# Performance work log

Measured on AMD Instinct MI355X. Metric: run time of the kernel, lower is better.

The kernel has to match this reference:

```python
import jax, jax.numpy as jnp
import numpy as np

B, N, D, H, K = 256, 196, 768, 256, 8
NEG = -1e9


def setup_inputs() -> dict:
    key = jax.random.key(0)
    ks = jax.random.split(key, 7)
    s_in = 1.0 / np.sqrt(D)
    s_h = 1.0 / np.sqrt(H)
    return {
        "region_features": jax.random.normal(ks[0], (B, N, D), dtype=jnp.float32),
        "Wn": jax.random.uniform(ks[1], (D, H), jnp.float32, -s_in, s_in),
        "bn": jax.random.uniform(ks[2], (H,), jnp.float32, -s_in, s_in),
        "Wm": jax.random.uniform(ks[3], (H, H), jnp.float32, -s_h, s_h),
        "bm": jax.random.uniform(ks[4], (H,), jnp.float32, -s_h, s_h),
        "Wo": jax.random.uniform(ks[5], (H, D), jnp.float32, -s_h, s_h),
        "bo": jax.random.uniform(ks[6], (D,), jnp.float32, -s_h, s_h),
    }


def reference(region_features, Wn, bn, Wm, bm, Wo, bo):
    b, n, d = region_features.shape
    h = Wn.shape[1]
    nodes = jnp.einsum("bnd,dh->bnh", region_features, Wn) + bn        # [B,N,H]
    sim = jnp.einsum("bnh,bmh->bnm", nodes, nodes)                      # [B,N,N]
    sim = sim + jnp.eye(n, dtype=sim.dtype) * NEG                       # mask self
    k = min(K, n - 1)
    topk_vals, topk_idx = jax.lax.top_k(sim, k)                         # [B,N,k]
    # gather neighbor node features: nodes[b, topk_idx[b,n,k]]
    flat_idx = topk_idx.reshape(b, n * k)                               # [B,N*k]
    neigh = jnp.take_along_axis(nodes, flat_idx[:, :, None], axis=1)    # [B,N*k,H]
    neighs = neigh.reshape(b, n, k, h).mean(axis=2)                     # [B,N,H]
    msgs = jax.nn.relu(jnp.einsum("bnh,hg->bng", neighs, Wm) + bm)      # [B,N,H]
    updated = nodes + msgs
    out = jnp.einsum("bnh,hd->bnd", updated, Wo) + bo                   # [B,N,D]
    return (out, topk_vals)
```

## Files before the change

### kernel.cpp

```cpp
#include <hip/hip_runtime.h>


#define NN 196
#define MM 208
#define DD 768
#define HH 256

typedef unsigned short u16;
typedef __attribute__((ext_vector_type(8))) short short8;
typedef __attribute__((ext_vector_type(4))) float f32x4;

#define GLD16(gp, lp) __builtin_amdgcn_global_load_lds( \
    (__attribute__((address_space(1))) const void*)(gp), \
    (__attribute__((address_space(3))) void*)(lp), 16, 0, 0)

__device__ __forceinline__ u16 f2b(float f) {
  union { float f; unsigned int i; } c; c.f = f;
  unsigned int x = c.i;
  return (u16)((x + 0x7fffu + ((x >> 16) & 1u)) >> 16);
}
__device__ __forceinline__ float b2f(u16 u) {
  union { float f; unsigned int i; } c; c.i = ((unsigned int)u) << 16; return c.f;
}

__global__ __launch_bounds__(256) void transpose_w(
    const float* __restrict__ in, u16* __restrict__ out, int R, int C)
{
  __shared__ u16 tile[32][33];
  int bx = blockIdx.x, by = blockIdx.y;
  int t = threadIdx.x;
  int i = t >> 5, j = t & 31;
  #pragma unroll
  for (int s = 0; s < 32; s += 8)
    tile[i + s][j] = f2b(in[(size_t)(by * 32 + i + s) * C + bx * 32 + j]);
  __syncthreads();
  #pragma unroll
  for (int s = 0; s < 32; s += 8)
    out[(size_t)(bx * 32 + i + s) * R + by * 32 + j] = tile[j][i + s];
}

__global__ __launch_bounds__(1024, 4) void fused_batch(
    const float* __restrict__ X, const u16* __restrict__ WnT,
    const float* __restrict__ bn, const u16* __restrict__ WmT,
    const float* __restrict__ bm, const u16* __restrict__ WoT,
    const float* __restrict__ bo, u16* __restrict__ updatedG,
    float* __restrict__ outG, float* __restrict__ valsG)
{
  extern __shared__ __align__(16) u16 smem[];
  u16* nodesS = smem;
  u16* Xbuf0 = smem + 53248;
  u16* Xbuf1 = smem + 53248 + 6656;
  float* simS0 = (float*)(smem + 53248);
  float* simS1 = (float*)(smem + 53248 + 6656);
  u16* neighS0 = smem + 53248 + 13312;
  u16* neighS1 = smem + 53248 + 13312 + 4096;

  const int t = threadIdx.x;
  const int w = t >> 6;
  const int lane = t & 63;
  const int l15 = lane & 15;
  const int kg = lane >> 4;
  const int b = blockIdx.x;
  const float* Xb = X + (size_t)b * (NN * DD);
  u16* updGb = updatedG + (size_t)b * MM * HH;

  f32x4 acc[13];
  #pragma unroll
  for (int fr = 0; fr < 13; ++fr) acc[fr] = (f32x4)0.0f;

  const bool xact = (t < 832);
  const int xrow = t >> 2;
  const int xr2 = (xrow < NN) ? xrow : (NN - 1);
  const int xcb = (t & 3) * 8;
  const int xsw = (xrow >> 1) & 3;
  const int xj0 = t & 3;

  f32x4 xsA[2], xsB[2], xsC[2];
  short8 bfrC0, bfrN0;

#define S1_ISSUE(SET, KT) do { \
    const float* xp_ = Xb + (size_t)xr2 * DD + (KT) * 32 + xcb; \
    SET[0] = *(const f32x4*)(xp_); SET[1] = *(const f32x4*)(xp_ + 4); \
  } while (0)

#define S1_COMMIT(SET, BUFW) do { \
    short8 v_; \
    _Pragma("unroll") for (int q_ = 0; q_ < 8; ++q_) v_[q_] = (short)f2b(SET[q_ >> 2][q_ & 3]); \
    *(short8*)((BUFW) + xrow * 32 + ((xj0 ^ xsw) << 3)) = v_; \
  } while (0)

#define S1_STEP(KT, XI, XC, BUFR, BUFW) do { \
    if (xact && (KT) + 3 < 24) S1_ISSUE(XI, (KT) + 3); \
    if ((KT) + 1 < 24) \
      bfrN0 = *(const short8*)(WnT + (size_t)(w * 16 + l15) * DD + ((KT) + 1) * 32 + kg * 8); \
    __builtin_amdgcn_s_setprio(1); \
    _Pragma("unroll") for (int fr_ = 0; fr_ < 13; ++fr_) { \
      const int r_ = fr_ * 16 + l15; \
      short8 a_ = *(const short8*)((BUFR) + r_ * 32 + ((kg ^ ((r_ >> 1) & 3)) << 3)); \
      acc[fr_] = __builtin_amdgcn_mfma_f32_16x16x32_bf16(a_, bfrC0, acc[fr_], 0, 0, 0); \
    } \
    __builtin_amdgcn_s_setprio(0); \
    if (xact && (KT) + 1 < 24) S1_COMMIT(XC, BUFW); \
    __syncthreads(); \
    bfrC0 = bfrN0; \
  } while (0)

  if (xact) { S1_ISSUE(xsA, 0); S1_ISSUE(xsB, 1); S1_ISSUE(xsC, 2); S1_COMMIT(xsA, Xbuf0); }
  bfrC0 = *(const short8*)(WnT + (size_t)(w * 16 + l15) * DD + kg * 8);
  __syncthreads();

  for (int kb = 0; kb < 24; kb += 6) {
    S1_STEP(kb + 0, xsA, xsB, Xbuf0, Xbuf1);
    S1_STEP(kb + 1, xsB, xsC, Xbuf1, Xbuf0);
    S1_STEP(kb + 2, xsC, xsA, Xbuf0, Xbuf1);
    S1_STEP(kb + 3, xsA, xsB, Xbuf1, Xbuf0);
    S1_STEP(kb + 4, xsB, xsC, Xbuf0, Xbuf1);
    S1_STEP(kb + 5, xsC, xsA, Xbuf1, Xbuf0);
  }

  {
    const float bnv = bn[w * 16 + l15];
    #pragma unroll
    for (int fr = 0; fr < 13; ++fr)
      #pragma unroll
      for (int ri = 0; ri < 4; ++ri) {
        const int r = fr * 16 + kg * 4 + ri;
        const int c = w * 16 + l15;
        nodesS[r * 256 + (((c >> 3) ^ (r & 7)) << 3) + (c & 7)] = f2b(acc[fr][ri] + bnv);
      }
  }
  __syncthreads();

  const float bmv = bm[w * 16 + l15];

  for (int s = 0; s < 13; ++s) {
    float* simSp = (s & 1) ? simS1 : simS0;
    u16* neighSp = (s & 1) ? neighS1 : neighS0;

    if (w < 13) {
      f32x4 s0 = (f32x4)0.0f;
      __builtin_amdgcn_s_setprio(1);
      #pragma unroll
      for (int kt = 0; kt < 8; ++kt) {
        const int ar = s * 16 + l15;
        const int ja = kt * 4 + kg;
        short8 av = *(const short8*)(nodesS + ar * 256 + ((ja ^ (ar & 7)) << 3));
        const int br = w * 16 + l15;
        short8 bv = *(const short8*)(nodesS + br * 256 + ((ja ^ (br & 7)) << 3));
        s0 = __builtin_amdgcn_mfma_f32_16x16x32_bf16(av, bv, s0, 0, 0, 0);
      }
      __builtin_amdgcn_s_setprio(0);
      #pragma unroll
      for (int ri = 0; ri < 4; ++ri) simSp[(kg * 4 + ri) * MM + w * 16 + l15] = s0[ri];
    }
    __syncthreads();

    {
      const int lr = w;
      const int n = s * 16 + lr;
      if (n < NN) {
        const float* srow = simSp + lr * MM;
        unsigned int v[4];
        #pragma unroll
        for (int i = 0; i < 4; ++i) {
          const int c = i * 64 + lane;
          const float f = (c < NN && c != n) ? srow[c] : -1e30f;
          union { float f; unsigned int i; } cv; cv.f = f;
          const unsigned int u = cv.i;
          const unsigned int key = u ^ ((u & 0x80000000u) ? 0xFFFFFFFFu : 0x80000000u);
          v[i] = (key & 0xFFFFFF00u) | (255u - (unsigned int)c);
        }
        int kcol[8];
        #pragma unroll
        for (int it = 0; it < 8; ++it) {
          unsigned int p0 = v[0] > v[1] ? v[0] : v[1];
          unsigned int p1 = v[2] > v[3] ? v[2] : v[3];
          unsigned int pk = p0 > p1 ? p0 : p1;
          #pragma unroll
          for (int off = 32; off >= 1; off >>= 1) {
            const unsigned int o = (unsigned int)__shfl_xor((int)pk, off);
            pk = o > pk ? o : pk;
          }
          const int cm = 255 - (int)(pk & 255u);
          kcol[it] = cm;
          if (lane == 0) {
            const unsigned int key = pk & 0xFFFFFF00u;
            union { float f; unsigned int i; } rv;
            rv.i = (key & 0x80000000u) ? (key ^ 0x80000000u) : ~key;
            valsG[((size_t)b * NN + n) * 8 + it] = rv.f;
          }
          if (lane == (cm & 63)) v[cm >> 6] = 0u;
        }
        float a0 = 0.f, a1 = 0.f, a2 = 0.f, a3 = 0.f;
        #pragma unroll
        for (int j = 0; j < 8; ++j) {
          const int kr = kcol[j];
          const uint2 u = *(const uint2*)(nodesS + kr * 256 + (((lane >> 1) ^ (kr & 7)) << 3) + (lane & 1) * 4);
          a0 += b2f((u16)(u.x & 0xffff)); a1 += b2f((u16)(u.x >> 16));
          a2 += b2f((u16)(u.y & 0xffff)); a3 += b2f((u16)(u.y >> 16));
        }
        const int jN = lane >> 1;
        u16* np = neighSp + lr * 256 + ((jN ^ (lr & 7)) << 3) + (lane & 1) * 4;
        np[0] = f2b(a0 * 0.125f); np[1] = f2b(a1 * 0.125f);
        np[2] = f2b(a2 * 0.125f); np[3] = f2b(a3 * 0.125f);
      }
    }
    __syncthreads();

    {
      f32x4 m0 = (f32x4)0.0f;
      __builtin_amdgcn_s_setprio(1);
      #pragma unroll
      for (int kt = 0; kt < 8; ++kt) {
        const int ja = kt * 4 + kg;
        short8 a = *(const short8*)(neighSp + l15 * 256 + ((ja ^ (l15 & 7)) << 3));
        short8 b0 = *(const short8*)(WmT + (size_t)(w * 16 + l15) * HH + kt * 32 + kg * 8);
        m0 = __builtin_amdgcn_mfma_f32_16x16x32_bf16(a, b0, m0, 0, 0, 0);
      }
      __builtin_amdgcn_s_setprio(0);
      #pragma unroll
      for (int ri = 0; ri < 4; ++ri) {
        const int r = s * 16 + kg * 4 + ri;
        const int c = w * 16 + l15;
        const float mv = m0[ri] + bmv;
        const float nodev = b2f(nodesS[r * 256 + (((c >> 3) ^ (r & 7)) << 3) + (c & 7)]);
        updGb[(size_t)r * HH + c] = f2b(nodev + fmaxf(mv, 0.0f));
      }
    }
  }

  __syncthreads();
  #pragma unroll
  for (int q = 0; q < 7; ++q) {
    const int si = q * 1024 + t;
    if (si < 6656) {
      const int r = si >> 5;
      const int jj = si & 31;
      const int j = jj ^ (r & 7);
      GLD16(updGb + (size_t)r * HH + j * 8, nodesS + si * 8);
    }
  }
  __syncthreads();

  for (int ch = 0; ch < 3; ++ch) {
    f32x4 oacc[13];
    #pragma unroll
    for (int fr = 0; fr < 13; ++fr) oacc[fr] = (f32x4)0.0f;
    __builtin_amdgcn_s_setprio(1);
    #pragma unroll
    for (int kt = 0; kt < 8; ++kt) {
      short8 bfr = *(const short8*)(WoT + (size_t)(ch * 256 + w * 16 + l15) * HH + kt * 32 + kg * 8);
      #pragma unroll
      for (int fr = 0; fr < 13; ++fr) {
        const int r = fr * 16 + l15;
        const int ja = kt * 4 + kg;
        short8 a = *(const short8*)(nodesS + r * 256 + ((ja ^ (r & 7)) << 3));
        oacc[fr] = __builtin_amdgcn_mfma_f32_16x16x32_bf16(a, bfr, oacc[fr], 0, 0, 0);
      }
    }
    __builtin_amdgcn_s_setprio(0);
    const float bov = bo[ch * 256 + w * 16 + l15];
    #pragma unroll
    for (int fr = 0; fr < 13; ++fr)
      #pragma unroll
      for (int ri = 0; ri < 4; ++ri) {
        const int r = fr * 16 + kg * 4 + ri;
        if (r < NN)
          outG[((size_t)b * NN + r) * DD + ch * 256 + w * 16 + l15] =
              oacc[fr][ri] + bov;
      }
  }
}

extern "C" void kernel_launch(void* const* d_in, const int* in_sizes, int n_in,
                              void* d_out, int out_size, void* d_ws, size_t ws_size,
                              hipStream_t stream) {
  const float* X  = (const float*)d_in[0];
  const float* Wn = (const float*)d_in[1];
  const float* bn = (const float*)d_in[2];
  const float* Wm = (const float*)d_in[3];
  const float* bm = (const float*)d_in[4];
  const float* Wo = (const float*)d_in[5];
  const float* bo = (const float*)d_in[6];

  char* p = (char*)d_ws;
  u16* WnT = (u16*)p;  p += (size_t)256 * 768 * 2;
  u16* WmT = (u16*)p;  p += (size_t)256 * 256 * 2;
  u16* WoT = (u16*)p;  p += (size_t)768 * 256 * 2;
  u16* updatedG = (u16*)p;  p += (size_t)256 * MM * HH * 2;

  float* out  = (float*)d_out;
  float* vals = out + (size_t)256 * NN * DD;

  transpose_w<<<dim3(256 / 32, 768 / 32), 256, 0, stream>>>(Wn, WnT, 768, 256);
  transpose_w<<<dim3(256 / 32, 256 / 32), 256, 0, stream>>>(Wm, WmT, 256, 256);
  transpose_w<<<dim3(768 / 32, 256 / 32), 256, 0, stream>>>(Wo, WoT, 256, 768);

  const int smem_bytes = 149504;
  (void)hipFuncSetAttribute((const void*)fused_batch,
                            hipFuncAttributeMaxDynamicSharedMemorySize, smem_bytes);
  fused_batch<<<256, 1024, smem_bytes, stream>>>(X, WnT, bn, WmT, bm, WoT, bo,
                                                 updatedG, out, vals);
}
```

Before: 169.9 us.

## Split fused batch kernel into nodes GEMM, graph strips, and output GEMM kernels

The single per-batch fused kernel is split into three launches: a node-projection GEMM writing bf16 nodes to global memory, a graph kernel that loads nodes, computes similarity/top-k/messages and writes the updated features, and a separate output GEMM that tiles 64-row slabs across 832 blocks. The aim is to stop one large, shared-memory-heavy, 256-block kernel from being limited by occupancy and serialization. Each phase can use its own shared-memory footprint, and the output projection gets more parallel blocks. In exchange, the nodes tensor takes an extra global write and read, and two more kernel launches are added.

```diff
diff --git a/kernel.cpp b/kernel.cpp
--- a/kernel.cpp
+++ b/kernel.cpp
@@ -39,21 +39,12 @@
     out[(size_t)(bx * 32 + i + s) * R + by * 32 + j] = tile[j][i + s];
 }
 
-__global__ __launch_bounds__(1024, 4) void fused_batch(
+__global__ __launch_bounds__(1024, 4) void nodes_gemm(
     const float* __restrict__ X, const u16* __restrict__ WnT,
-    const float* __restrict__ bn, const u16* __restrict__ WmT,
-    const float* __restrict__ bm, const u16* __restrict__ WoT,
-    const float* __restrict__ bo, u16* __restrict__ updatedG,
-    float* __restrict__ outG, float* __restrict__ valsG)
+    const float* __restrict__ bn, u16* __restrict__ nodesG)
 {
-  extern __shared__ __align__(16) u16 smem[];
-  u16* nodesS = smem;
-  u16* Xbuf0 = smem + 53248;
-  u16* Xbuf1 = smem + 53248 + 6656;
-  float* simS0 = (float*)(smem + 53248);
-  float* simS1 = (float*)(smem + 53248 + 6656);
-  u16* neighS0 = smem + 53248 + 13312;
-  u16* neighS1 = smem + 53248 + 13312 + 4096;
+  __shared__ __align__(16) u16 Xbuf0[6656];
+  __shared__ __align__(16) u16 Xbuf1[6656];
 
   const int t = threadIdx.x;
   const int w = t >> 6;
@@ -62,7 +53,6 @@
   const int kg = lane >> 4;
   const int b = blockIdx.x;
   const float* Xb = X + (size_t)b * (NN * DD);
-  u16* updGb = updatedG + (size_t)b * MM * HH;
 
   f32x4 acc[13];
   #pragma unroll
@@ -119,6 +109,7 @@
   }
 
   {
+    u16* ndst = nodesG + (size_t)b * (MM * HH);
     const float bnv = bn[w * 16 + l15];
     #pragma unroll
     for (int fr = 0; fr < 13; ++fr)
@@ -126,8 +117,41 @@
       for (int ri = 0; ri < 4; ++ri) {
         const int r = fr * 16 + kg * 4 + ri;
         const int c = w * 16 + l15;
-        nodesS[r * 256 + (((c >> 3) ^ (r & 7)) << 3) + (c & 7)] = f2b(acc[fr][ri] + bnv);
-      }
+        ndst[(size_t)r * HH + c] = f2b(acc[fr][ri] + bnv);
+      }
+  }
+}
+
+__global__ __launch_bounds__(1024, 4) void graph_strips(
+    const u16* __restrict__ nodesG, const u16* __restrict__ WmT,
+    const float* __restrict__ bm, u16* __restrict__ updatedG,
+    float* __restrict__ valsG)
+{
+  extern __shared__ __align__(16) u16 smem[];
+  u16* nodesS = smem;
+  float* simS0 = (float*)(smem + 53248);
+  float* simS1 = (float*)(smem + 53248 + 6656);
+  u16* neighS0 = smem + 53248 + 13312;
+  u16* neighS1 = smem + 53248 + 13312 + 4096;
+
+  const int t = threadIdx.x;
+  const int w = t >> 6;
+  const int lane = t & 63;
+  const int l15 = lane & 15;
+  const int kg = lane >> 4;
+  const int b = blockIdx.x;
+  const u16* nodesGb = nodesG + (size_t)b * (MM * HH);
+  u16* updGb = updatedG + (size_t)b * MM * HH;
+
+  #pragma unroll
+  for (int q = 0; q < 7; ++q) {
+    const int si = q * 1024 + t;
+    if (si < 6656) {
+      const int r = si >> 5;
+      const int jj = si & 31;
+      const int j = jj ^ (r & 7);
+      GLD16(nodesGb + (size_t)r * HH + j * 8, nodesS + si * 8);
+    }
   }
   __syncthreads();
 
@@ -228,45 +252,58 @@
       }
     }
   }
-
+}
+
+__global__ __launch_bounds__(1024, 8) void out_gemm(
+    const u16* __restrict__ updatedG, const u16* __restrict__ WoT,
+    const float* __restrict__ bo, float* __restrict__ outG)
+{
+  __shared__ __align__(16) u16 aS[64 * 256];
+
+  const int t = threadIdx.x;
+  const int w = t >> 6;
+  const int lane = t & 63;
+  const int l15 = lane & 15;
+  const int kg = lane >> 4;
+  const int row0 = blockIdx.x * 64;
+
+  #pragma unroll
+  for (int q = 0; q < 2; ++q) {
+    const int si = q * 1024 + t;
+    const int r = si >> 5;
+    const int jj = si & 31;
+    const int j = jj ^ (r & 7);
+    GLD16(updatedG + (size_t)(row0 + r) * HH + j * 8, aS + si * 8);
+  }
   __syncthreads();
-  #pragma unroll
-  for (int q = 0; q < 7; ++q) {
-    const int si = q * 1024 + t;
-    if (si < 6656) {
-      const int r = si >> 5;
-      const int jj = si & 31;
-      const int j = jj ^ (r & 7);
-      GLD16(updGb + (size_t)r * HH + j * 8, nodesS + si * 8);
-    }
-  }
-  __syncthreads();
 
   for (int ch = 0; ch < 3; ++ch) {
-    f32x4 oacc[13];
+    f32x4 oacc[4];
     #pragma unroll
-    for (int fr = 0; fr < 13; ++fr) oacc[fr] = (f32x4)0.0f;
+    for (int fr = 0; fr < 4; ++fr) oacc[fr] = (f32x4)0.0f;
     __builtin_amdgcn_s_setprio(1);
     #pragma unroll
     for (int kt = 0; kt < 8; ++kt) {
       short8 bfr = *(const short8*)(WoT + (size_t)(ch * 256 + w * 16 + l15) * HH + kt * 32 + kg * 8);
       #pragma unroll
-      for (int fr = 0; fr < 13; ++fr) {
+      for (int fr = 0; fr < 4; ++fr) {
         const int r = fr * 16 + l15;
         const int ja = kt * 4 + kg;
-        short8 a = *(const short8*)(nodesS + r * 256 + ((ja ^ (r & 7)) << 3));
+        short8 a = *(const short8*)(aS + r * 256 + ((ja ^ (r & 7)) << 3));
         oacc[fr] = __builtin_amdgcn_mfma_f32_16x16x32_bf16(a, bfr, oacc[fr], 0, 0, 0);
       }
     }
     __builtin_amdgcn_s_setprio(0);
     const float bov = bo[ch * 256 + w * 16 + l15];
     #pragma unroll
-    for (int fr = 0; fr < 13; ++fr)
+    for (int fr = 0; fr < 4; ++fr)
       #pragma unroll
       for (int ri = 0; ri < 4; ++ri) {
-        const int r = fr * 16 + kg * 4 + ri;
-        if (r < NN)
-          outG[((size_t)b * NN + r) * DD + ch * 256 + w * 16 + l15] =
+        const int rg = row0 + fr * 16 + kg * 4 + ri;
+        const int batch = rg / MM;
+        const int rl = rg - batch * MM;
+        if (rl < NN)
+          outG[((size_t)batch * NN + rl) * DD + ch * 256 + w * 16 + l15] =
               oacc[fr][ri] + bov;
       }
   }
@@ -287,6 +324,7 @@
   u16* WnT = (u16*)p;  p += (size_t)256 * 768 * 2;
   u16* WmT = (u16*)p;  p += (size_t)256 * 256 * 2;
   u16* WoT = (u16*)p;  p += (size_t)768 * 256 * 2;
+  u16* nodesG = (u16*)p;    p += (size_t)256 * MM * HH * 2;
   u16* updatedG = (u16*)p;  p += (size_t)256 * MM * HH * 2;
 
   float* out  = (float*)d_out;
@@ -296,9 +334,12 @@
   transpose_w<<<dim3(256 / 32, 256 / 32), 256, 0, stream>>>(Wm, WmT, 256, 256);
   transpose_w<<<dim3(768 / 32, 256 / 32), 256, 0, stream>>>(Wo, WoT, 256, 768);
 
+  nodes_gemm<<<256, 1024, 0, stream>>>(X, WnT, bn, nodesG);
+
   const int smem_bytes = 149504;
-  (void)hipFuncSetAttribute((const void*)fused_batch,
+  (void)hipFuncSetAttribute((const void*)graph_strips,
                             hipFuncAttributeMaxDynamicSharedMemorySize, smem_bytes);
-  fused_batch<<<256, 1024, smem_bytes, stream>>>(X, WnT, bn, WmT, bm, WoT, bo,
-                                                 updatedG, out, vals);
-}
+  graph_strips<<<256, 1024, smem_bytes, stream>>>(nodesG, WmT, bm, updatedG, vals);
+
+  out_gemm<<<832, 1024, 0, stream>>>(updatedG, WoT, bo, out);
+}
```

Result: slower. 517.3 us (+204.4%).

## Hoist sim B-fragments into registers and re-tile output GEMM by row blocks

Applied to the files above, without the earlier changes.

The similarity loop's B operand, which is the same for a given wave across all 13 row steps, is now loaded from LDS once into registers instead of every iteration. The output projection is reorganised so each of 13 waves owns a 16-row block of updated nodes, held in registers, and sweeps all 768 output columns in pairs of 16-column tiles. That second change removes the repeated LDS A-operand reads of the old column-split scheme, but it reads Wo from global memory per wave, leaves 3 of the 16 waves idle, and adds register pressure.

```diff
diff --git a/kernel.cpp b/kernel.cpp
--- a/kernel.cpp
+++ b/kernel.cpp
@@ -133,6 +133,16 @@
 
   const float bmv = bm[w * 16 + l15];
 
+  short8 bvh[8];
+  if (w < 13) {
+    const int br = w * 16 + l15;
+    #pragma unroll
+    for (int kt = 0; kt < 8; ++kt) {
+      const int ja = kt * 4 + kg;
+      bvh[kt] = *(const short8*)(nodesS + br * 256 + ((ja ^ (br & 7)) << 3));
+    }
+  }
+
   for (int s = 0; s < 13; ++s) {
     float* simSp = (s & 1) ? simS1 : simS0;
     u16* neighSp = (s & 1) ? neighS1 : neighS0;
@@ -145,9 +155,7 @@
         const int ar = s * 16 + l15;
         const int ja = kt * 4 + kg;
         short8 av = *(const short8*)(nodesS + ar * 256 + ((ja ^ (ar & 7)) << 3));
-        const int br = w * 16 + l15;
-        short8 bv = *(const short8*)(nodesS + br * 256 + ((ja ^ (br & 7)) << 3));
-        s0 = __builtin_amdgcn_mfma_f32_16x16x32_bf16(av, bv, s0, 0, 0, 0);
+        s0 = __builtin_amdgcn_mfma_f32_16x16x32_bf16(av, bvh[kt], s0, 0, 0, 0);
       }
       __builtin_amdgcn_s_setprio(0);
       #pragma unroll
@@ -242,33 +250,42 @@
   }
   __syncthreads();
 
-  for (int ch = 0; ch < 3; ++ch) {
-    f32x4 oacc[13];
-    #pragma unroll
-    for (int fr = 0; fr < 13; ++fr) oacc[fr] = (f32x4)0.0f;
-    __builtin_amdgcn_s_setprio(1);
-    #pragma unroll
-    for (int kt = 0; kt < 8; ++kt) {
-      short8 bfr = *(const short8*)(WoT + (size_t)(ch * 256 + w * 16 + l15) * HH + kt * 32 + kg * 8);
-      #pragma unroll
-      for (int fr = 0; fr < 13; ++fr) {
-        const int r = fr * 16 + l15;
-        const int ja = kt * 4 + kg;
-        short8 a = *(const short8*)(nodesS + r * 256 + ((ja ^ (r & 7)) << 3));
-        oacc[fr] = __builtin_amdgcn_mfma_f32_16x16x32_bf16(a, bfr, oacc[fr], 0, 0, 0);
-      }
-    }
-    __builtin_amdgcn_s_setprio(0);
-    const float bov = bo[ch * 256 + w * 16 + l15];
-    #pragma unroll
-    for (int fr = 0; fr < 13; ++fr)
+  if (w < 13) {
+    short8 avh[8];
+    {
+      const int r = w * 16 + l15;
+      #pragma unroll
+      for (int kt = 0; kt < 8; ++kt)
+        avh[kt] = *(const short8*)(nodesS + r * 256 + (((kt * 4 + kg) ^ (r & 7)) << 3));
+    }
+    const int orow = w * 16 + kg * 4;
+    float* outRowBase = outG + (size_t)b * NN * DD;
+
+    for (int ct2 = 0; ct2 < 24; ++ct2) {
+      const int c0 = ct2 * 32 + l15;
+      const int c1 = c0 + 16;
+      f32x4 acc0 = (f32x4)0.0f, acc1 = (f32x4)0.0f;
+      __builtin_amdgcn_s_setprio(1);
+      #pragma unroll
+      for (int kt = 0; kt < 8; ++kt) {
+        short8 b0 = *(const short8*)(WoT + (size_t)c0 * HH + kt * 32 + kg * 8);
+        short8 b1 = *(const short8*)(WoT + (size_t)c1 * HH + kt * 32 + kg * 8);
+        acc0 = __builtin_amdgcn_mfma_f32_16x16x32_bf16(avh[kt], b0, acc0, 0, 0, 0);
+        acc1 = __builtin_amdgcn_mfma_f32_16x16x32_bf16(avh[kt], b1, acc1, 0, 0, 0);
+      }
+      __builtin_amdgcn_s_setprio(0);
+      const float bo0 = bo[c0];
+      const float bo1 = bo[c1];
       #pragma unroll
       for (int ri = 0; ri < 4; ++ri) {
-        const int r = fr * 16 + kg * 4 + ri;
-        if (r < NN)
-          outG[((size_t)b * NN + r) * DD + ch * 256 + w * 16 + l15] =
-              oacc[fr][ri] + bov;
-      }
+        const int r = orow + ri;
+        if (r < NN) {
+          float* op = outRowBase + (size_t)r * DD + ct2 * 32 + l15;
+          op[0]  = acc0[ri] + bo0;
+          op[16] = acc1[ri] + bo1;
+        }
+      }
+    }
   }
 }
 
```

Measured after the change: 279.7 us. +64.6%, slower.

## Fuse output projection into per-strip message loop via LDS instead of global roundtrip

Applied to the files above, without the earlier changes.

Each 16-row strip's updated node features are now written to a small swizzled LDS buffer instead of a global workspace. The output projection (Wo GEMM) for that strip runs immediately inside the strip loop. Each wave covers three 16-column output tiles, so the separate reload phase and the final 3-chunk GEMM are gone. This removes the global write/readback of the updated tensor and two block barriers. The cost is an extra barrier per strip, more LDS, and Wo fragments reloaded from global memory for every strip rather than once per chunk.

```diff
diff --git a/kernel.cpp b/kernel.cpp
--- a/kernel.cpp
+++ b/kernel.cpp
@@ -9,10 +9,6 @@
 typedef unsigned short u16;
 typedef __attribute__((ext_vector_type(8))) short short8;
 typedef __attribute__((ext_vector_type(4))) float f32x4;
-
-#define GLD16(gp, lp) __builtin_amdgcn_global_load_lds( \
-    (__attribute__((address_space(1))) const void*)(gp), \
-    (__attribute__((address_space(3))) void*)(lp), 16, 0, 0)
 
 __device__ __forceinline__ u16 f2b(float f) {
   union { float f; unsigned int i; } c; c.f = f;
@@ -43,7 +39,7 @@
     const float* __restrict__ X, const u16* __restrict__ WnT,
     const float* __restrict__ bn, const u16* __restrict__ WmT,
     const float* __restrict__ bm, const u16* __restrict__ WoT,
-    const float* __restrict__ bo, u16* __restrict__ updatedG,
+    const float* __restrict__ bo,
     float* __restrict__ outG, float* __restrict__ valsG)
 {
   extern __shared__ __align__(16) u16 smem[];
@@ -54,6 +50,7 @@
   float* simS1 = (float*)(smem + 53248 + 6656);
   u16* neighS0 = smem + 53248 + 13312;
   u16* neighS1 = smem + 53248 + 13312 + 4096;
+  u16* updS    = smem + 53248 + 13312 + 8192;
 
   const int t = threadIdx.x;
   const int w = t >> 6;
@@ -62,7 +59,6 @@
   const int kg = lane >> 4;
   const int b = blockIdx.x;
   const float* Xb = X + (size_t)b * (NN * DD);
-  u16* updGb = updatedG + (size_t)b * MM * HH;
 
   f32x4 acc[13];
   #pragma unroll
@@ -221,54 +217,43 @@
       #pragma unroll
       for (int ri = 0; ri < 4; ++ri) {
         const int r = s * 16 + kg * 4 + ri;
+        const int rl = kg * 4 + ri;
         const int c = w * 16 + l15;
         const float mv = m0[ri] + bmv;
         const float nodev = b2f(nodesS[r * 256 + (((c >> 3) ^ (r & 7)) << 3) + (c & 7)]);
-        updGb[(size_t)r * HH + c] = f2b(nodev + fmaxf(mv, 0.0f));
-      }
-    }
-  }
-
-  __syncthreads();
-  #pragma unroll
-  for (int q = 0; q < 7; ++q) {
-    const int si = q * 1024 + t;
-    if (si < 6656) {
-      const int r = si >> 5;
-      const int jj = si & 31;
-      const int j = jj ^ (r & 7);
-      GLD16(updGb + (size_t)r * HH + j * 8, nodesS + si * 8);
-    }
-  }
-  __syncthreads();
-
-  for (int ch = 0; ch < 3; ++ch) {
-    f32x4 oacc[13];
-    #pragma unroll
-    for (int fr = 0; fr < 13; ++fr) oacc[fr] = (f32x4)0.0f;
-    __builtin_amdgcn_s_setprio(1);
-    #pragma unroll
-    for (int kt = 0; kt < 8; ++kt) {
-      short8 bfr = *(const short8*)(WoT + (size_t)(ch * 256 + w * 16 + l15) * HH + kt * 32 + kg * 8);
-      #pragma unroll
-      for (int fr = 0; fr < 13; ++fr) {
-        const int r = fr * 16 + l15;
+        updS[rl * 256 + (((c >> 3) ^ (rl & 7)) << 3) + (c & 7)] = f2b(nodev + fmaxf(mv, 0.0f));
+      }
+    }
+    __syncthreads();
+
+    {
+      short8 avh2[8];
+      #pragma unroll
+      for (int kt = 0; kt < 8; ++kt) {
         const int ja = kt * 4 + kg;
-        short8 a = *(const short8*)(nodesS + r * 256 + ((ja ^ (r & 7)) << 3));
-        oacc[fr] = __builtin_amdgcn_mfma_f32_16x16x32_bf16(a, bfr, oacc[fr], 0, 0, 0);
-      }
-    }
-    __builtin_amdgcn_s_setprio(0);
-    const float bov = bo[ch * 256 + w * 16 + l15];
-    #pragma unroll
-    for (int fr = 0; fr < 13; ++fr)
-      #pragma unroll
-      for (int ri = 0; ri < 4; ++ri) {
-        const int r = fr * 16 + kg * 4 + ri;
-        if (r < NN)
-          outG[((size_t)b * NN + r) * DD + ch * 256 + w * 16 + l15] =
-              oacc[fr][ri] + bov;
-      }
+        avh2[kt] = *(const short8*)(updS + l15 * 256 + ((ja ^ (l15 & 7)) << 3));
+      }
+      const int rg0 = s * 16 + kg * 4;
+      #pragma unroll
+      for (int i = 0; i < 3; ++i) {
+        const int col = (w * 3 + i) * 16 + l15;
+        f32x4 oa = (f32x4)0.0f;
+        __builtin_amdgcn_s_setprio(1);
+        #pragma unroll
+        for (int kt = 0; kt < 8; ++kt) {
+          short8 bfr = *(const short8*)(WoT + (size_t)col * HH + kt * 32 + kg * 8);
+          oa = __builtin_amdgcn_mfma_f32_16x16x32_bf16(avh2[kt], bfr, oa, 0, 0, 0);
+        }
+        __builtin_amdgcn_s_setprio(0);
+        const float bov = bo[col];
+        #pragma unroll
+        for (int ri = 0; ri < 4; ++ri) {
+          const int r = rg0 + ri;
+          if (r < NN)
+            outG[((size_t)b * NN + r) * DD + col] = oa[ri] + bov;
+        }
+      }
+    }
   }
 }
 
@@ -287,7 +272,6 @@
   u16* WnT = (u16*)p;  p += (size_t)256 * 768 * 2;
   u16* WmT = (u16*)p;  p += (size_t)256 * 256 * 2;
   u16* WoT = (u16*)p;  p += (size_t)768 * 256 * 2;
-  u16* updatedG = (u16*)p;  p += (size_t)256 * MM * HH * 2;
 
   float* out  = (float*)d_out;
   float* vals = out + (size_t)256 * NN * DD;
@@ -296,9 +280,9 @@
   transpose_w<<<dim3(256 / 32, 256 / 32), 256, 0, stream>>>(Wm, WmT, 256, 256);
   transpose_w<<<dim3(768 / 32, 256 / 32), 256, 0, stream>>>(Wo, WoT, 256, 768);
 
-  const int smem_bytes = 149504;
+  const int smem_bytes = 157696;
   (void)hipFuncSetAttribute((const void*)fused_batch,
                             hipFuncAttributeMaxDynamicSharedMemorySize, smem_bytes);
   fused_batch<<<256, 1024, smem_bytes, stream>>>(X, WnT, bn, WmT, bm, WoT, bo,
-                                                 updatedG, out, vals);
-}
+                                                 out, vals);
+}
```

Result: slower. 328.1 us (+93.0%).
